# Kernel optimization log

Measured on AMD Instinct MI355X. Metric: run time of the kernel, lower is better.

## Reference

```python
import jax, jax.numpy as jnp
import numpy as np
from jax.scipy.special import logsumexp

NEG = -1e30  # stand-in for -inf that is safe under fp32 and vjp
MAX_SEG_LEN = 64
WITH_TRANSITION = True


def setup_inputs() -> dict:
    key = jax.random.key(0)
    k1, k2 = jax.random.split(key)
    B, S, L = 8, 512, 32
    segment_score = jax.random.normal(k1, (B, S, S, L), dtype=jnp.float32)
    transitions = jax.random.uniform(k2, (L, L), dtype=jnp.float32)  # matches nn.init.uniform_(0,1)
    return {"segment_score": segment_score, "transitions": transitions}


def _compute_log_z(segment_score, transitions, max_seg_len=MAX_SEG_LEN, with_transition=WITH_TRANSITION):
    # segment_score: [B, S, S, L] (start, end, label); transitions: [L, L]
    B, S, _, L = segment_score.shape
    M = max_seg_len
    dt = segment_score.dtype
    diag = jnp.diagonal(transitions)  # [L]

    # alpha_pad slot (p + M) holds log_alpha at frame p; slots < M act as -inf guard
    alpha_pad = jnp.full((B, S + M, L), NEG, dtype=dt)
    alpha_pad = alpha_pad.at[:, M, :].set(segment_score[:, 0, 0, :])

    w = jnp.arange(M)
    j = (M - w).astype(dt)  # window slot w corresponds to segment length j = M - w
    # transition term for a continuation segment of length j ending in label cur, coming from prev:
    # T[prev, cur] + diag[cur] * (j - 1)   -> [M, prev, cur]
    trans_term = transitions[None, :, :] + diag[None, None, :] * (j[:, None, None] - 1.0)

    def step(alpha_pad, f_end):
        # segment scores for all segments ending at f_end: [B, S, L]
        seg_col = jax.lax.dynamic_index_in_dim(segment_score, f_end, axis=2, keepdims=False)
        # pad so window slot w maps to start position f_end - M + 1 + w (length j = M - w)
        seg_pad = jnp.pad(seg_col, ((0, 0), (M - 1, 0), (0, 0)))
        seg_win = jax.lax.dynamic_slice_in_dim(seg_pad, f_end, M, axis=1)     # [B, M, L]
        # alpha window slot w -> frame f_end - M + w = f_end - j (guarded by NEG padding)
        alpha_win = jax.lax.dynamic_slice_in_dim(alpha_pad, f_end, M, axis=1)  # [B, M, L]

        # continuation scores: alpha[prev] + seg * j (+ transition)  -> [B, M, prev, cur]
        scores = alpha_win[:, :, :, None] + (seg_win * j[None, :, None])[:, :, None, :]
        if with_transition:
            scores = scores + trans_term[None, :, :, :]

        # initial segment [0, f_end] (no predecessor), only valid while f_end + 1 <= M
        f = f_end.astype(dt)
        init = seg_col[:, 0, :] * (f + 1.0)
        if with_transition:
            init = init + diag[None, :] * f
        init = jnp.where(f_end < M, init, NEG)

        all_scores = jnp.concatenate([scores.reshape(B, M * L, L), init[:, None, :]], axis=1)
        new_alpha = logsumexp(all_scores, axis=1)  # [B, L]

        alpha_pad = jax.lax.dynamic_update_slice_in_dim(
            alpha_pad, new_alpha[:, None, :], f_end + M, axis=1)
        return alpha_pad, None

    alpha_pad, _ = jax.lax.scan(step, alpha_pad, jnp.arange(1, S))
    log_z = logsumexp(alpha_pad[:, S - 1 + M, :], axis=1)  # [B]
    return log_z


def reference(segment_score, transitions):
    return _compute_log_z(segment_score, transitions)
```

## Files before the change

kernel.cpp:

```cpp
#include <hip/hip_runtime.h>

#define NEGF (-1e30f)

constexpr int S = 512;
constexpr int L = 32;
constexpr int SL1 = (S + 1) * L;
constexpr int SLN = S * L;
constexpr int SSL = S * S * L;
constexpr int RSTR = 33;
constexpr int RROWS = 128;
constexpr int RWRAP = RROWS * RSTR;
constexpr int SPIN_CAP = 1 << 20;


template <int CTRL>
__device__ __forceinline__ float dppf(float x) {
    return __builtin_bit_cast(float,
        __builtin_amdgcn_update_dpp(0, __builtin_bit_cast(int, x),
                                    CTRL, 0xf, 0xf, true));
}
#define RED32_MAX(v) do { v = fmaxf(v, dppf<0xB1>(v));                      \
                          v = fmaxf(v, dppf<0x4E>(v));                      \
                          v = fmaxf(v, dppf<0x141>(v));                     \
                          v = fmaxf(v, dppf<0x140>(v));                     \
                          v = fmaxf(v, __shfl_xor(v, 16)); } while (0)

#define CHAIN(ff_, SBUF, DOPOLL, DOPUB) do {                                \
    const int ff = (ff_);                                                   \
       \
    float tj[14];                                                           \
    _Pragma("unroll")                                                       \
    for (int i = 0; i < 14; ++i)                                            \
        tj[i] = bH[i] + fmaf(SBUF[i + 1], (float)(i + 2), dgc[i]);          \
    float Mp = fmaxf(pp1.x, tj[0]);                                         \
    _Pragma("unroll")                                                       \
    for (int i = 1; i < 14; ++i) Mp = fmaxf(Mp, tj[i]);                     \
    float Sp = pp1.y * __expf(pp1.x - Mp);                                  \
    _Pragma("unroll")                                                       \
    for (int i = 0; i < 14; ++i) Sp += __expf(tj[i] - Mp);                  \
    float mxn = Ma;                                                         \
    RED32_MAX(mxn);                     \
                               \
    const float uu = Sa * __expf(Ma - mx);                                  \
    if (t < 32) ubuf[c] = uu;                                               \
    const float4 u0 = *(const float4*)&ubuf[0];                             \
    const float4 u1 = *(const float4*)&ubuf[4];                             \
    const float4 u2 = *(const float4*)&ubuf[8];                             \
    const float4 u3 = *(const float4*)&ubuf[12];                            \
    const float4 u4 = *(const float4*)&ubuf[16];                            \
    const float4 u5 = *(const float4*)&ubuf[20];                            \
    const float4 u6 = *(const float4*)&ubuf[24];                            \
    const float4 u7 = *(const float4*)&ubuf[28];                            \
    float d0 = u0.x * E[0];                                                 \
    d0 = fmaf(u0.y, E[1], d0);  d0 = fmaf(u0.z, E[2], d0);                  \
    d0 = fmaf(u0.w, E[3], d0);  d0 = fmaf(u1.x, E[4], d0);                  \
    d0 = fmaf(u1.y, E[5], d0);  d0 = fmaf(u1.z, E[6], d0);                  \
    d0 = fmaf(u1.w, E[7], d0);                                              \
    float d1 = u2.x * E[8];                                                 \
    d1 = fmaf(u2.y, E[9],  d1); d1 = fmaf(u2.z, E[10], d1);                 \
    d1 = fmaf(u2.w, E[11], d1); d1 = fmaf(u3.x, E[12], d1);                 \
    d1 = fmaf(u3.y, E[13], d1); d1 = fmaf(u3.z, E[14], d1);                 \
    d1 = fmaf(u3.w, E[15], d1);                                             \
    float d2 = u4.x * E[16];                                                \
    d2 = fmaf(u4.y, E[17], d2); d2 = fmaf(u4.z, E[18], d2);                 \
    d2 = fmaf(u4.w, E[19], d2); d2 = fmaf(u5.x, E[20], d2);                 \
    d2 = fmaf(u5.y, E[21], d2); d2 = fmaf(u5.z, E[22], d2);                 \
    d2 = fmaf(u5.w, E[23], d2);                                             \
    float d3 = u6.x * E[24];                                                \
    d3 = fmaf(u6.y, E[25], d3); d3 = fmaf(u6.z, E[26], d3);                 \
    d3 = fmaf(u6.w, E[27], d3); d3 = fmaf(u7.x, E[28], d3);                 \
    d3 = fmaf(u7.y, E[29], d3); d3 = fmaf(u7.z, E[30], d3);                 \
    d3 = fmaf(u7.w, E[31], d3);                                             \
    const float dot = (d0 + d1) + (d2 + d3);                                \
    const float bb = mx + __logf(dot);                                      \
    if (t < 32) ring[wadr] = bb;                                            \
    wadr += RSTR; if (wadr >= RWRAP) wadr -= RWRAP;                         \
                                                  \
    const float t1 = bb + SBUF[0];                                          \
    const float Man = fmaxf(Mp, t1);                                        \
    Sa = fmaf(Sp, __expf(Mp - Man), __expf(t1 - Man));                      \
    Ma = Man;                                                               \
    mx = mxn;                                                               \
    if (DOPUB) {                                                            \
        asm volatile("s_waitcnt lgkmcnt(0)" ::: "memory");                  \
        if (t == 0) cntv[3] = ff;                                           \
    }                                                                       \
    if (DOPOLL) {                                                           \
        const int Fb = ff + 3;                                              \
        if (Fb <= 508) {                                                    \
            volatile int* cw = &cntv[(Fb >> 2) % 3];                        \
            int zz = 0;                                                     \
            while (*cw < Fb && ++zz < SPIN_CAP) {}                          \
            __builtin_amdgcn_fence(__ATOMIC_ACQUIRE, "workgroup", "local"); \
        }                                                                   \
    }                                                                       \
    pp1 = pp2;                                                              \
    pp2 = part[(ff + 3) & 31][c];                                           \
    _Pragma("unroll")                                                       \
    for (int i = 13; i > 0; --i) bH[i] = bH[i - 1];                         \
    bH[0] = bb;                                                             \
             \
    _Pragma("unroll")                                                       \
    for (int i = 0; i < 15; ++i) {                                          \
        int o = offv[i];                                                    \
        o = (o < (int)c || o >= SSL) ? (int)c : o;    \
        SBUF[i] = segB[o];                                                  \
        offv[i] += SL1;                                                     \
    }                                                                       \
} while (0)

#define LLOAD(BUF) do {                                                     \
    _Pragma("unroll")                                                       \
    for (int i = 0; i < 25; ++i) {                                          \
        int o = offs[i];                                                    \
        o = (o < (int)c || o >= SSL) ? (int)c : o;                          \
        BUF[i] = segB[o];                                                   \
        offs[i] += SL1;                                                     \
    }                                                                       \
} while (0)

#define LFRAME(ff_, BUF, MSK) do {                                          \
    const int ff = (ff_);                                                   \
    float tt[25];                                                           \
    _Pragma("unroll")                                                       \
    for (int i = 0; i < 25; ++i) {                                          \
        const float rv = ring[radr[i]];                                     \
        const float tv = rv + fmaf(BUF[i], jfv[i], dgv[i]);                 \
        bool vld = (i < nt);                                                \
        if (MSK) vld = vld && (jlo + i <= ff + 1);                          \
        tt[i] = vld ? tv : NEGF;                                            \
        radr[i] += RSTR;                                                    \
        if (radr[i] >= RWRAP) radr[i] -= RWRAP;                             \
    }                                                                       \
    float m = tt[0];                                                        \
    _Pragma("unroll")                                                       \
    for (int i = 1; i < 25; ++i) m = fmaxf(m, tt[i]);                       \
    float s = 0.f;                                                          \
    _Pragma("unroll")                                                       \
    for (int i = 0; i < 25; ++i) s += __expf(tt[i] - m);                    \
    const float m2 = __shfl_xor(m, 32);                                     \
    const float s2 = __shfl_xor(s, 32);                                     \
    const float Mw = fmaxf(m, m2);                                          \
    const float Sw = fmaf(s, __expf(m - Mw), s2 * __expf(m2 - Mw));         \
    if (h == 0) part[ff & 31][c] = make_float2(Mw, Sw);                     \
} while (0)

__launch_bounds__(256, 1)
__global__ void semicrf_fwd(const float* __restrict__ seg,
                            const float* __restrict__ trans,
                            float* __restrict__ out)
{
    const int t  = threadIdx.x;
    const int b  = blockIdx.x;
    const int c  = t & 31;
    const int h  = (t >> 5) & 1;
    const int wv = t >> 6;

    __shared__ float ring[RROWS * RSTR];
    __shared__ float2 part[32][32];
    __shared__ __align__(16) float ubuf[32];
    __shared__ int cnt_s[4];

    if (t < 32) ring[t] = 0.f;
    if (t < 4)  cnt_s[t] = -1;
    __syncthreads();

    const float* segB = seg + (size_t)b * S * S * L;
    volatile int* cntv = cnt_s;

    if (wv == 0) {
        __builtin_amdgcn_s_setprio(1);
        float E[32];
#pragma unroll
        for (int i = 0; i < 32; ++i) E[i] = __expf(trans[i * 32 + c]);
        const float diag_c = trans[c * 33];
        float dgc[14];
#pragma unroll
        for (int i = 0; i < 14; ++i) dgc[i] = diag_c * (float)(i + 1);

        float bH[14];
        bH[0] = 0.f;
#pragma unroll
        for (int i = 1; i < 14; ++i) bH[i] = NEGF;

        float sO[15], sE[15];
        int offv[15];
#pragma unroll
        for (int i = 0; i < 15; ++i) {
            const int j = i + 1;
            int o1 = 1 * SL1 - (j - 1) * SLN + (int)c;
            int o2 = 2 * SL1 - (j - 1) * SLN + (int)c;
            o1 = o1 < (int)c ? (int)c : o1;
            o2 = o2 < (int)c ? (int)c : o2;
            sO[i] = segB[o1];
            sE[i] = segB[o2];
            offv[i] = 3 * SL1 - (j - 1) * SLN + (int)c;
        }

        float Ma = segB[c];
        float Sa = 1.f;
        float mx = Ma;
        RED32_MAX(mx);
        int wadr = RSTR + (int)c;

        {
            volatile int* cw = &cntv[0];
            int zz = 0;
            while (*cw < 0 && ++zz < SPIN_CAP) {}
            __builtin_amdgcn_fence(__ATOMIC_ACQUIRE, "workgroup", "local");
        }
        float2 pp1 = part[1][c];
        float2 pp2 = part[2][c];

        for (int f = 0; f < 508; f += 4) {
            CHAIN(f + 0, sO, false, false);
            CHAIN(f + 1, sE, true,  false);
            CHAIN(f + 2, sO, false, false);
            CHAIN(f + 3, sE, false, true);
        }
        CHAIN(508, sO, false, false);
        CHAIN(509, sE, true,  false);
        CHAIN(510, sO, false, false);

        float m = Ma + __logf(Sa);
        float ss = 1.f;
#pragma unroll
        for (int mk = 1; mk <= 16; mk <<= 1) {
            const float m2 = __shfl_xor(m, mk);
            const float s2 = __shfl_xor(ss, mk);
            const float mn = fmaxf(m, m2);
            ss = ss * __expf(m - mn) + s2 * __expf(m2 - mn);
            m  = mn;
        }
        if (t == 0) out[b] = m + __logf(ss);
    } else {
        const int wl  = wv - 1;
        const int jlo = h ? 41 : 16;
        const int nt  = h ? 24 : 25;
        const float diag_c = trans[c * 33];

        float jfv[25], dgv[25];
        int offs[25], radr[25];
        const int F0 = 4 * wl;
#pragma unroll
        for (int i = 0; i < 25; ++i) {
            const int j = jlo + i;
            jfv[i] = (float)j;
            dgv[i] = diag_c * (float)(j - 1);
            offs[i] = F0 * SL1 - (j - 1) * SLN + (int)c;
            const int row = (F0 - j + 1) & (RROWS - 1);
            radr[i] = row * RSTR + (int)c;
        }

        float bufA[25], bufB[25];
        int cdv = -1;
        int F = F0;
        LLOAD(bufA);
        LLOAD(bufB);
        while (F <= 508) {
            if (F >= 16) {
                const int need = F - 13;
                int zz = 0;
                while (cdv < need && ++zz < SPIN_CAP) {
                    __builtin_amdgcn_s_sleep(1); cdv = cntv[3];
                }
                __builtin_amdgcn_fence(__ATOMIC_ACQUIRE, "workgroup", "local");
            }
            if (F <= 60) {
                LFRAME(F + 0, bufA, true);  LLOAD(bufA);
                LFRAME(F + 1, bufB, true);  LLOAD(bufB);
                LFRAME(F + 2, bufA, true);
                LFRAME(F + 3, bufB, true);
            } else {
                LFRAME(F + 0, bufA, false); LLOAD(bufA);
                LFRAME(F + 1, bufB, false); LLOAD(bufB);
                LFRAME(F + 2, bufA, false);
                LFRAME(F + 3, bufB, false);
            }
            asm volatile("s_waitcnt lgkmcnt(0)" ::: "memory");
            if ((t & 63) == 0) cntv[wl] = F;
#pragma unroll
            for (int i = 0; i < 25; ++i) offs[i] += 8 * SL1;
#pragma unroll
            for (int i = 0; i < 25; ++i) {
                radr[i] += 8 * RSTR;
                if (radr[i] >= RWRAP) radr[i] -= RWRAP;
            }
            F += 12;
            if (F <= 508) { LLOAD(bufA); LLOAD(bufB); }
        }
    }
}

extern "C" void kernel_launch(void* const* d_in, const int* in_sizes, int n_in,
                              void* d_out, int out_size, void* d_ws, size_t ws_size,
                              hipStream_t stream) {
    const float* seg   = (const float*)d_in[0];
    const float* trans = (const float*)d_in[1];
    float* out = (float*)d_out;
    hipLaunchKernelGGL(semicrf_fwd, dim3(8), dim3(256), 0, stream,
                       seg, trans, out);
}
```

Measured before the change: 646.2 us.

## Unroll chain by 16 with rotating history, tree reductions, and batched ring loads

The serial chain wave now runs 16-step unrolled bodies. The history buffer becomes a 16-slot register array indexed modulo 16 instead of being shifted every step, and four segment-prefetch buffers replace two, giving each load more lead time. Max and sum reductions in both the chain and the helper waves use balanced trees instead of linear chains, which shortens dependency depth. Helper waves load 28 ring values once per group of four frames instead of doing per-element wrapped address updates for each frame. The part array is also initialised, and the t<32 guards on shared writes are removed. The cost is higher register pressure from the extra buffers and larger unrolled code.

```diff
diff --git a/kernel.cpp b/kernel.cpp
--- a/kernel.cpp
+++ b/kernel.cpp
@@ -25,24 +25,31 @@
                           v = fmaxf(v, dppf<0x140>(v));                     \
                           v = fmaxf(v, __shfl_xor(v, 16)); } while (0)
 
-#define CHAIN(ff_, SBUF, DOPOLL, DOPUB) do {                                \
-    const int ff = (ff_);                                                   \
-       \
+#define CHAIN(U, SBUF, DOPOLL, DOPUB) do {                                  \
+    const int ff = fbase + (U);                                             \
+                     \
     float tj[14];                                                           \
     _Pragma("unroll")                                                       \
     for (int i = 0; i < 14; ++i)                                            \
-        tj[i] = bH[i] + fmaf(SBUF[i + 1], (float)(i + 2), dgc[i]);          \
-    float Mp = fmaxf(pp1.x, tj[0]);                                         \
-    _Pragma("unroll")                                                       \
-    for (int i = 1; i < 14; ++i) Mp = fmaxf(Mp, tj[i]);                     \
-    float Sp = pp1.y * __expf(pp1.x - Mp);                                  \
-    _Pragma("unroll")                                                       \
-    for (int i = 0; i < 14; ++i) Sp += __expf(tj[i] - Mp);                  \
+        tj[i] = bH[((U) + 14 - i) & 15] +                                   \
+                fmaf(SBUF[i + 1], (float)(i + 2), dgc[i]);                  \
+    float Mp = fmaxf(                                                       \
+        fmaxf(fmaxf(fmaxf(tj[0],tj[1]),fmaxf(tj[2],tj[3])),                 \
+              fmaxf(fmaxf(tj[4],tj[5]),fmaxf(tj[6],tj[7]))),                \
+        fmaxf(fmaxf(fmaxf(tj[8],tj[9]),fmaxf(tj[10],tj[11])),               \
+              fmaxf(fmaxf(tj[12],tj[13]), pp1.x)));                         \
+    float exv[14];                                                          \
+    _Pragma("unroll")                                                       \
+    for (int i = 0; i < 14; ++i) exv[i] = __expf(tj[i] - Mp);               \
+    const float exP = pp1.y * __expf(pp1.x - Mp);                           \
+    const float Sp =                                                        \
+        (((exv[0]+exv[1])+(exv[2]+exv[3]))+((exv[4]+exv[5])+(exv[6]+exv[7])))\
+      + (((exv[8]+exv[9])+(exv[10]+exv[11]))+((exv[12]+exv[13])+exP));      \
     float mxn = Ma;                                                         \
     RED32_MAX(mxn);                     \
                                \
     const float uu = Sa * __expf(Ma - mx);                                  \
-    if (t < 32) ubuf[c] = uu;                                               \
+    ubuf[c] = uu;                      \
     const float4 u0 = *(const float4*)&ubuf[0];                             \
     const float4 u1 = *(const float4*)&ubuf[4];                             \
     const float4 u2 = *(const float4*)&ubuf[8];                             \
@@ -73,7 +80,7 @@
     d3 = fmaf(u7.w, E[31], d3);                                             \
     const float dot = (d0 + d1) + (d2 + d3);                                \
     const float bb = mx + __logf(dot);                                      \
-    if (t < 32) ring[wadr] = bb;                                            \
+    ring[wadr] = bb;                       \
     wadr += RSTR; if (wadr >= RWRAP) wadr -= RWRAP;                         \
                                                   \
     const float t1 = bb + SBUF[0];                                          \
@@ -81,6 +88,7 @@
     Sa = fmaf(Sp, __expf(Mp - Man), __expf(t1 - Man));                      \
     Ma = Man;                                                               \
     mx = mxn;                                                               \
+    bH[(U) & 15] = bb;                                                      \
     if (DOPUB) {                                                            \
         asm volatile("s_waitcnt lgkmcnt(0)" ::: "memory");                  \
         if (t == 0) cntv[3] = ff;                                           \
@@ -96,17 +104,25 @@
     }                                                                       \
     pp1 = pp2;                                                              \
     pp2 = part[(ff + 3) & 31][c];                                           \
-    _Pragma("unroll")                                                       \
-    for (int i = 13; i > 0; --i) bH[i] = bH[i - 1];                         \
-    bH[0] = bb;                                                             \
-             \
+       \
     _Pragma("unroll")                                                       \
     for (int i = 0; i < 15; ++i) {                                          \
         int o = offv[i];                                                    \
-        o = (o < (int)c || o >= SSL) ? (int)c : o;    \
+        o = (o < (int)c || o >= SSL) ? (int)c : o;                          \
         SBUF[i] = segB[o];                                                  \
         offv[i] += SL1;                                                     \
     }                                                                       \
+} while (0)
+
+#define BODY16() do {                                                       \
+    CHAIN(0, sA, 0,0); CHAIN(1, sB, 1,0);                                   \
+    CHAIN(2, sC, 0,0); CHAIN(3, sD, 0,1);                                   \
+    CHAIN(4, sA, 0,0); CHAIN(5, sB, 1,0);                                   \
+    CHAIN(6, sC, 0,0); CHAIN(7, sD, 0,1);                                   \
+    CHAIN(8, sA, 0,0); CHAIN(9, sB, 1,0);                                   \
+    CHAIN(10,sC, 0,0); CHAIN(11,sD, 0,1);                                   \
+    CHAIN(12,sA, 0,0); CHAIN(13,sB, 1,0);                                   \
+    CHAIN(14,sC, 0,0); CHAIN(15,sD, 0,1);                                   \
 } while (0)
 
 #define LLOAD(BUF) do {                                                     \
@@ -119,25 +135,42 @@
     }                                                                       \
 } while (0)
 
-#define LFRAME(ff_, BUF, MSK) do {                                          \
-    const int ff = (ff_);                                                   \
+#define LOADBR() do {                                                       \
+    _Pragma("unroll")                                                       \
+    for (int k = 0; k < 28; ++k) {                                          \
+        int a = rbase + k * RSTR;                                           \
+        if (a >= RWRAP) a -= RWRAP;                                         \
+        bR[k] = ring[a];                                                    \
+    }                                                                       \
+} while (0)
+
+#define LF(q_, BUF, MSK) do {                                               \
+    const int ff = F + (q_);                                                \
     float tt[25];                                                           \
     _Pragma("unroll")                                                       \
     for (int i = 0; i < 25; ++i) {                                          \
-        const float rv = ring[radr[i]];                                     \
-        const float tv = rv + fmaf(BUF[i], jfv[i], dgv[i]);                 \
+        const float tv = bR[(q_) + 24 - i] + fmaf(BUF[i], jfv[i], dgv[i]);  \
         bool vld = (i < nt);                                                \
         if (MSK) vld = vld && (jlo + i <= ff + 1);                          \
         tt[i] = vld ? tv : NEGF;                                            \
-        radr[i] += RSTR;                                                    \
-        if (radr[i] >= RWRAP) radr[i] -= RWRAP;                             \
-    }                                                                       \
-    float m = tt[0];                                                        \
-    _Pragma("unroll")                                                       \
-    for (int i = 1; i < 25; ++i) m = fmaxf(m, tt[i]);                       \
-    float s = 0.f;                                                          \
-    _Pragma("unroll")                                                       \
-    for (int i = 0; i < 25; ++i) s += __expf(tt[i] - m);                    \
+    }                                                                       \
+    float m = fmaxf(                                                        \
+        fmaxf(fmaxf(fmaxf(tt[0],tt[1]),fmaxf(tt[2],tt[3])),                 \
+              fmaxf(fmaxf(tt[4],tt[5]),fmaxf(tt[6],tt[7]))),                \
+        fmaxf(fmaxf(fmaxf(tt[8],tt[9]),fmaxf(tt[10],tt[11])),               \
+              fmaxf(fmaxf(tt[12],tt[13]),fmaxf(tt[14],tt[15]))));           \
+    m = fmaxf(m, fmaxf(                                                     \
+        fmaxf(fmaxf(tt[16],tt[17]),fmaxf(tt[18],tt[19])),                   \
+        fmaxf(fmaxf(tt[20],tt[21]),fmaxf(tt[22],tt[23]))));                 \
+    m = fmaxf(m, tt[24]);                                                   \
+    float e_[25];                                                           \
+    _Pragma("unroll")                                                       \
+    for (int i = 0; i < 25; ++i) e_[i] = __expf(tt[i] - m);                 \
+    const float s =                                                         \
+        ((((e_[0]+e_[1])+(e_[2]+e_[3]))+((e_[4]+e_[5])+(e_[6]+e_[7])))      \
+       + (((e_[8]+e_[9])+(e_[10]+e_[11]))+((e_[12]+e_[13])+(e_[14]+e_[15]))))\
+      + ((((e_[16]+e_[17])+(e_[18]+e_[19]))+((e_[20]+e_[21])+(e_[22]+e_[23])))\
+       + e_[24]);                                                           \
     const float m2 = __shfl_xor(m, 32);                                     \
     const float s2 = __shfl_xor(s, 32);                                     \
     const float Mw = fmaxf(m, m2);                                          \
@@ -161,6 +194,8 @@
     __shared__ __align__(16) float ubuf[32];
     __shared__ int cnt_s[4];
 
+    for (int i = t; i < 32 * 32; i += 256)
+        ((float2*)part)[i] = make_float2(NEGF, 0.f);
     if (t < 32) ring[t] = 0.f;
     if (t < 4)  cnt_s[t] = -1;
     __syncthreads();
@@ -178,23 +213,28 @@
 #pragma unroll
         for (int i = 0; i < 14; ++i) dgc[i] = diag_c * (float)(i + 1);
 
-        float bH[14];
-        bH[0] = 0.f;
-#pragma unroll
-        for (int i = 1; i < 14; ++i) bH[i] = NEGF;
-
-        float sO[15], sE[15];
+        float bH[16];
+#pragma unroll
+        for (int i = 0; i < 16; ++i) bH[i] = NEGF;
+        bH[15] = 0.f;
+
+        float sA[15], sB[15], sC[15], sD[15];
         int offv[15];
 #pragma unroll
         for (int i = 0; i < 15; ++i) {
-            const int j = i + 1;
-            int o1 = 1 * SL1 - (j - 1) * SLN + (int)c;
-            int o2 = 2 * SL1 - (j - 1) * SLN + (int)c;
+            int o1 = 1 * SL1 - i * SLN + (int)c;
+            int o2 = 2 * SL1 - i * SLN + (int)c;
+            int o3 = 3 * SL1 - i * SLN + (int)c;
+            int o4 = 4 * SL1 - i * SLN + (int)c;
             o1 = o1 < (int)c ? (int)c : o1;
             o2 = o2 < (int)c ? (int)c : o2;
-            sO[i] = segB[o1];
-            sE[i] = segB[o2];
-            offv[i] = 3 * SL1 - (j - 1) * SLN + (int)c;
+            o3 = o3 < (int)c ? (int)c : o3;
+            o4 = o4 < (int)c ? (int)c : o4;
+            sA[i] = segB[o1];
+            sB[i] = segB[o2];
+            sC[i] = segB[o3];
+            sD[i] = segB[o4];
+            offv[i] = 5 * SL1 - i * SLN + (int)c;
         }
 
         float Ma = segB[c];
@@ -212,15 +252,20 @@
         float2 pp1 = part[1][c];
         float2 pp2 = part[2][c];
 
-        for (int f = 0; f < 508; f += 4) {
-            CHAIN(f + 0, sO, false, false);
-            CHAIN(f + 1, sE, true,  false);
-            CHAIN(f + 2, sO, false, false);
-            CHAIN(f + 3, sE, false, true);
-        }
-        CHAIN(508, sO, false, false);
-        CHAIN(509, sE, true,  false);
-        CHAIN(510, sO, false, false);
+        int fbase = 0;
+        BODY16();
+#pragma unroll 1
+        for (fbase = 16; fbase <= 480; fbase += 16)
+            BODY16();
+        fbase = 496;
+        CHAIN(0, sA, 0,0); CHAIN(1, sB, 1,0);
+        CHAIN(2, sC, 0,0); CHAIN(3, sD, 0,1);
+        CHAIN(4, sA, 0,0); CHAIN(5, sB, 1,0);
+        CHAIN(6, sC, 0,0); CHAIN(7, sD, 0,1);
+        CHAIN(8, sA, 0,0); CHAIN(9, sB, 1,0);
+        CHAIN(10,sC, 0,0); CHAIN(11,sD, 0,1);
+        CHAIN(12,sA, 0,0); CHAIN(13,sB, 1,0);
+        CHAIN(14,sC, 0,0);
 
         float m = Ma + __logf(Sa);
         float ss = 1.f;
@@ -237,22 +282,22 @@
         const int wl  = wv - 1;
         const int jlo = h ? 41 : 16;
         const int nt  = h ? 24 : 25;
+        const int jhi = h ? 65 : 40;
         const float diag_c = trans[c * 33];
 
         float jfv[25], dgv[25];
-        int offs[25], radr[25];
+        int offs[25];
         const int F0 = 4 * wl;
 #pragma unroll
         for (int i = 0; i < 25; ++i) {
-            const int j = jlo + i;
-            jfv[i] = (float)j;
-            dgv[i] = diag_c * (float)(j - 1);
-            offs[i] = F0 * SL1 - (j - 1) * SLN + (int)c;
-            const int row = (F0 - j + 1) & (RROWS - 1);
-            radr[i] = row * RSTR + (int)c;
-        }
-
-        float bufA[25], bufB[25];
+            const int jj = jlo + i;
+            jfv[i] = (float)jj;
+            dgv[i] = diag_c * (float)(jj - 1);
+            offs[i] = F0 * SL1 - (jj - 1) * SLN + (int)c;
+        }
+        int rbase = (((F0 - jhi + 1) & 127) * RSTR) + (int)c;
+
+        float bufA[25], bufB[25], bR[28];
         int cdv = -1;
         int F = F0;
         LLOAD(bufA);
@@ -266,26 +311,23 @@
                 }
                 __builtin_amdgcn_fence(__ATOMIC_ACQUIRE, "workgroup", "local");
             }
+            LOADBR();
             if (F <= 60) {
-                LFRAME(F + 0, bufA, true);  LLOAD(bufA);
-                LFRAME(F + 1, bufB, true);  LLOAD(bufB);
-                LFRAME(F + 2, bufA, true);
-                LFRAME(F + 3, bufB, true);
+                LF(0, bufA, 1); LLOAD(bufA);
+                LF(1, bufB, 1); LLOAD(bufB);
+                LF(2, bufA, 1);
+                LF(3, bufB, 1);
             } else {
-                LFRAME(F + 0, bufA, false); LLOAD(bufA);
-                LFRAME(F + 1, bufB, false); LLOAD(bufB);
-                LFRAME(F + 2, bufA, false);
-                LFRAME(F + 3, bufB, false);
+                LF(0, bufA, 0); LLOAD(bufA);
+                LF(1, bufB, 0); LLOAD(bufB);
+                LF(2, bufA, 0);
+                LF(3, bufB, 0);
             }
             asm volatile("s_waitcnt lgkmcnt(0)" ::: "memory");
             if ((t & 63) == 0) cntv[wl] = F;
 #pragma unroll
             for (int i = 0; i < 25; ++i) offs[i] += 8 * SL1;
-#pragma unroll
-            for (int i = 0; i < 25; ++i) {
-                radr[i] += 8 * RSTR;
-                if (radr[i] >= RWRAP) radr[i] -= RWRAP;
-            }
+            rbase += 12 * RSTR; if (rbase >= RWRAP) rbase -= RWRAP;
             F += 12;
             if (F <= 508) { LLOAD(bufA); LLOAD(bufB); }
         }
```

Result: slower. 752.1 us (+16.4%).
